# Kernel optimization log

Hardware: AMD Instinct MI355X
Metric: run time of the kernel (lower is better)

Reference implementation:

```python
import jax, jax.numpy as jnp
import numpy as np

N_NODES = 50000
N_EDGES = 400000
F_IN = 70
E_DIM = 4
HID = 128
HEADS = 4


def _add_self_loops(src, dst, edge_attr, n):
    # PyG GATConv(add_self_loops=True, fill_value='mean' when edge_dim is set):
    # self-loop edge_attr = per-dst-node mean of incoming edge_attr.
    cnt = jax.ops.segment_sum(jnp.ones((src.shape[0],), edge_attr.dtype), dst, n)
    loop_attr = jax.ops.segment_sum(edge_attr, dst, n) / jnp.clip(cnt, 1.0)[:, None]
    loop = jnp.arange(n, dtype=src.dtype)
    return (jnp.concatenate([src, loop]), jnp.concatenate([dst, loop]),
            jnp.concatenate([edge_attr, loop_attr], axis=0))


def _gat_layer(x, src, dst, e_attr, W, a_src, a_dst, We, a_edge, b, concat):
    # W: [in, H*D]; a_src/a_dst/a_edge: [H, D]; We: [edge_dim, H*D]
    n = x.shape[0]
    H, D = a_src.shape
    xs = (x @ W).reshape(n, H, D)                      # [N,H,D]
    s_src = jnp.einsum('nhd,hd->nh', xs, a_src)        # [N,H]
    s_dst = jnp.einsum('nhd,hd->nh', xs, a_dst)
    ee = (e_attr @ We).reshape(-1, H, D)               # [E,H,D]
    s_edge = jnp.einsum('ehd,hd->eh', ee, a_edge)
    alpha = jax.nn.leaky_relu(s_src[src] + s_dst[dst] + s_edge, 0.2)  # [E,H]
    # segment softmax over edges grouped by destination node
    m = jax.ops.segment_max(alpha, dst, n)
    m = jnp.where(jnp.isfinite(m), m, 0.0)
    ex = jnp.exp(alpha - m[dst])
    denom = jax.ops.segment_sum(ex, dst, n)
    alpha = ex / (denom[dst] + 1e-16)
    msg = xs[src] * alpha[..., None]                   # [E,H,D] -- dominant traffic
    agg = jax.ops.segment_sum(msg, dst, n)             # [N,H,D]
    out = agg.reshape(n, H * D) if concat else agg.mean(axis=1)
    return out + b


def _layer_norm(x, g, b, eps=1e-5):
    mu = x.mean(-1, keepdims=True)
    var = ((x - mu) ** 2).mean(-1, keepdims=True)
    return (x - mu) * jax.lax.rsqrt(var + eps) * g + b


def setup_inputs() -> dict:
    key = jax.random.key(0)
    ks = jax.random.split(key, 24)
    f32 = jnp.float32
    node_features = jax.random.normal(ks[0], (N_NODES, F_IN), f32)
    edge_index = jax.random.randint(ks[1], (2, N_EDGES), 0, N_NODES, jnp.int32)
    edge_attr = jax.random.uniform(ks[2], (N_EDGES, E_DIM), f32)
    s = 0.1
    return {
        'node_features': node_features,
        'edge_index': edge_index,
        'edge_attr': edge_attr,
        'W1': jax.random.normal(ks[3], (F_IN, HEADS * HID), f32) * s,
        'as1': jax.random.normal(ks[4], (HEADS, HID), f32) * s,
        'ad1': jax.random.normal(ks[5], (HEADS, HID), f32) * s,
        'We1': jax.random.normal(ks[6], (E_DIM, HEADS * HID), f32) * s,
        'ae1': jax.random.normal(ks[7], (HEADS, HID), f32) * s,
        'b1': jnp.zeros((HEADS * HID,), f32),
        # GAT layer 2: 512 -> 128, 1 head, mean
        'W2': jax.random.normal(ks[8], (HEADS * HID, HID), f32) * s,
        'as2': jax.random.normal(ks[9], (1, HID), f32) * s,
        'ad2': jax.random.normal(ks[10], (1, HID), f32) * s,
        'We2': jax.random.normal(ks[11], (E_DIM, HID), f32) * s,
        'ae2': jax.random.normal(ks[12], (1, HID), f32) * s,
        'b2': jnp.zeros((HID,), f32),
        'ln_g': jnp.ones((HID,), f32),
        'ln_b': jnp.zeros((HID,), f32),
        'pw': jax.random.normal(ks[13], (HID, 8), f32) * s,
        'pb': jnp.zeros((8,), f32),
        'dw': jax.random.normal(ks[14], (HID, 4), f32) * s,
        'db': jnp.zeros((4,), f32),
    }


def reference(node_features, edge_index, edge_attr, W1, as1, ad1, We1, ae1, b1,
              W2, as2, ad2, We2, ae2, b2, ln_g, ln_b, pw, pb, dw, db):
    n = node_features.shape[0]
    src, dst, ea = _add_self_loops(edge_index[0], edge_index[1], edge_attr, n)
    x = jax.nn.gelu(_gat_layer(node_features, src, dst, ea, W1, as1, ad1, We1, ae1, b1, True), approximate=False)
    x = jax.nn.gelu(_gat_layer(x, src, dst, ea, W2, as2, ad2, We2, ae2, b2, False), approximate=False)
    x = _layer_norm(x, ln_g, ln_b)
    return (x @ pw + pb, x @ dw + db)
```

## Files before the change

kernel.cpp:

```cpp
#include <hip/hip_runtime.h>
#include <hip/hip_bf16.h>
#include <math.h>

#define NN 50000
#define NE 400000
#define FIN 70
#define EDIM 4
#define HIDD 128
#define NHEAD 4
constexpr int ET = NE + NN;
constexpr int KP1 = 96;
constexpr int NFP = 72;
constexpr int SCB = (NN + 255) / 256;

constexpr size_t al4(size_t x){ return (x + 3) & ~size_t(3); }
constexpr size_t CNT_O   = 0;
constexpr size_t ZEND    = al4(CNT_O + NN);
constexpr size_t CSR_O   = ZEND;
constexpr size_t BSUM_O  = al4(CSR_O + NN + 1);
constexpr size_t BOFF_O  = al4(BSUM_O + 256);
constexpr size_t EPK_O   = al4(BOFF_O + 256);
constexpr size_t EXF1_O  = al4(EPK_O + (size_t)ET*4);
constexpr size_t EXF2_O  = al4(EXF1_O + (size_t)ET*4);
constexpr size_t SS1_O   = al4(EXF2_O + ET);
constexpr size_t SD1_O   = al4(SS1_O + (size_t)NN*4);
constexpr size_t SS2_O   = al4(SD1_O + (size_t)NN*4);
constexpr size_t SD2_O   = al4(SS2_O + NN);
constexpr size_t CST_O   = al4(SD2_O + NN);
constexpr size_t W1T_O   = al4(CST_O + 2048);
constexpr size_t W2T_O   = al4(W1T_O + 4*128*KP1/2);
constexpr size_t NFB_O   = al4(W2T_O + 128*512/2);
constexpr size_t AGG_O   = al4(NFB_O + (size_t)NN*NFP/2);
constexpr size_t XS2_O   = al4(AGG_O + (size_t)4*NN*KP1/2);

constexpr int VS1 = 0;
constexpr int VD1 = 320;
constexpr int VE1 = 640;
constexpr int VE2 = 656;
constexpr int VS2 = 704;
constexpr int VD2 = 1216;

typedef short s8v __attribute__((ext_vector_type(8)));
typedef float f4v __attribute__((ext_vector_type(4)));

__device__ __forceinline__ unsigned short f2b(float v){
  __hip_bfloat16 b = __float2bfloat16(v);
  return *(unsigned short*)&b;
}
__device__ __forceinline__ float b2f(unsigned u_lo16){
  return __uint_as_float(u_lo16 << 16);
}
__device__ __forceinline__ unsigned pk2(float lo, float hi){
  return (unsigned)f2b(lo) | ((unsigned)f2b(hi) << 16);
}
__device__ __forceinline__ float lrelu(float x){ return x > 0.f ? x : 0.2f * x; }

__device__ __forceinline__ float gelu_fast(float x){
  float z = x * 0.70710678118654752440f;
  float a = fabsf(z);
  float t = 1.f / (1.f + 0.3275911f * a);
  float p = ((((1.061405429f*t - 1.453152027f)*t + 1.421413741f)*t
              - 0.284496736f)*t + 0.254829592f)*t;
  float erfv = 1.f - p * __expf(-a * a);
  erfv = copysignf(erfv, z);
  return 0.5f * x * (1.f + erfv);
}

__global__ void k_deg(const int* __restrict__ ei, int* __restrict__ cnt){
  int e = blockIdx.x * 256 + threadIdx.x;
  if (e >= NE) return;
  atomicAdd(&cnt[ei[NE + e]], 1);
}

__global__ void k_scan1(const int* __restrict__ cnt, int* __restrict__ bsum){
  __shared__ int ws[4];
  int t = threadIdx.x, lane = t & 63, w = t >> 6;
  int i = blockIdx.x * 256 + t;
  int v = (i < NN) ? cnt[i] + 1 : 0;
  for (int o = 32; o; o >>= 1) v += __shfl_down(v, o);
  if (lane == 0) ws[w] = v;
  __syncthreads();
  if (t == 0) bsum[blockIdx.x] = ws[0] + ws[1] + ws[2] + ws[3];
}

__global__ void k_scan2(const int* __restrict__ bsum, int* __restrict__ boff){
  __shared__ int ws[4];
  int t = threadIdx.x, lane = t & 63, w = t >> 6;
  int v = (t < SCB) ? bsum[t] : 0;
  int x = v;
  #pragma unroll
  for (int o = 1; o < 64; o <<= 1){ int u = __shfl_up(x, o); if (lane >= o) x += u; }
  if (lane == 63) ws[w] = x;
  __syncthreads();
  if (w == 0 && lane < 4){
    int y = ws[lane];
    #pragma unroll
    for (int o = 1; o < 4; o <<= 1){ int u = __shfl_up(y, o); if (lane >= o) y += u; }
    ws[lane] = y;
  }
  __syncthreads();
  int incl = x + (w > 0 ? ws[w - 1] : 0);
  if (t < SCB) boff[t] = incl - v;
}

__global__ void k_scan3(const int* __restrict__ cnt, const int* __restrict__ boff,
                        int* __restrict__ csr){
  __shared__ int ws[4];
  int t = threadIdx.x, lane = t & 63, w = t >> 6;
  int i = blockIdx.x * 256 + t;
  int v = (i < NN) ? cnt[i] + 1 : 0;
  int x = v;
  #pragma unroll
  for (int o = 1; o < 64; o <<= 1){ int u = __shfl_up(x, o); if (lane >= o) x += u; }
  if (lane == 63) ws[w] = x;
  __syncthreads();
  if (w == 0 && lane < 4){
    int y = ws[lane];
    #pragma unroll
    for (int o = 1; o < 4; o <<= 1){ int u = __shfl_up(y, o); if (lane >= o) y += u; }
    ws[lane] = y;
  }
  __syncthreads();
  if (i < NN) csr[i + 1] = boff[blockIdx.x] + (w > 0 ? ws[w - 1] : 0) + x;
  if (i == 0) csr[0] = 0;
}

__global__ void k_fill(const int* __restrict__ ei, const float* __restrict__ ea,
                       const int* __restrict__ csr, int* __restrict__ cnt,
                       int4* __restrict__ epk, const float* __restrict__ ss1,
                       const float* __restrict__ sd1, const float* __restrict__ C,
                       float4* __restrict__ exf){
  int e = blockIdx.x * 256 + threadIdx.x;
  if (e >= NE) return;
  int s = ei[e], d = ei[NE + e];
  int r = atomicSub(&cnt[d], 1);
  int p = csr[d] + r - 1;
  float4 a = *(const float4*)&ea[(size_t)e * 4];
  epk[p] = make_int4(s, d, (int)pk2(a.x, a.y), (int)pk2(a.z, a.w));
  float4 ssv = *(const float4*)&ss1[(size_t)s * 4];
  float4 sdv = *(const float4*)&sd1[(size_t)d * 4];
  float e0 = __expf(lrelu(ssv.x + sdv.x + a.x*C[VE1+0] + a.y*C[VE1+4] + a.z*C[VE1+8]  + a.w*C[VE1+12]));
  float e1 = __expf(lrelu(ssv.y + sdv.y + a.x*C[VE1+1] + a.y*C[VE1+5] + a.z*C[VE1+9]  + a.w*C[VE1+13]));
  float e2 = __expf(lrelu(ssv.z + sdv.z + a.x*C[VE1+2] + a.y*C[VE1+6] + a.z*C[VE1+10] + a.w*C[VE1+14]));
  float e3 = __expf(lrelu(ssv.w + sdv.w + a.x*C[VE1+3] + a.y*C[VE1+7] + a.z*C[VE1+11] + a.w*C[VE1+15]));
  exf[p] = make_float4(e0, e1, e2, e3);
}

__global__ void k_prep(const float* __restrict__ W1, const float* __restrict__ as1,
                       const float* __restrict__ ad1, const float* __restrict__ We1,
                       const float* __restrict__ ae1, const float* __restrict__ W2,
                       const float* __restrict__ as2, const float* __restrict__ ad2,
                       const float* __restrict__ We2, const float* __restrict__ ae2,
                       float* __restrict__ C){
  int t = threadIdx.x;
  if (t < 280){
    int k = t >> 2, h = t & 3;
    float s = 0.f, d = 0.f;
    for (int dd = 0; dd < 128; ++dd){
      float w = W1[k*512 + h*128 + dd];
      s += w * as1[h*128 + dd];
      d += w * ad1[h*128 + dd];
    }
    C[VS1 + t] = s; C[VD1 + t] = d;
  }
  if (t < 16){
    int k = t >> 2, h = t & 3;
    float s = 0.f;
    for (int dd = 0; dd < 128; ++dd) s += We1[k*512 + h*128 + dd] * ae1[h*128 + dd];
    C[VE1 + t] = s;
  }
  if (t < 4){
    float s = 0.f;
    for (int dd = 0; dd < 128; ++dd) s += We2[t*128 + dd] * ae2[dd];
    C[VE2 + t] = s;
  }
  {
    float s = 0.f, d = 0.f;
    for (int dd = 0; dd < 128; ++dd){
      float w = W2[t*128 + dd];
      s += w * as2[dd];
      d += w * ad2[dd];
    }
    C[VS2 + t] = s; C[VD2 + t] = d;
  }
}

__global__ void k_tw(const float* __restrict__ W1, const float* __restrict__ W2,
                     unsigned short* __restrict__ W1p, unsigned short* __restrict__ W2p){
  int i = blockIdx.x * 256 + threadIdx.x;
  if (i < 12*128*32){
    int kk = i & 31, r = (i >> 5) & 127, ph = i >> 12;
    int h = ph / 3, kf = ph - 3*h;
    int kg = kf*32 + kk;
    float v = (kg < FIN) ? W1[kg*512 + h*128 + r] : 0.f;
    W1p[i] = f2b(v);
  } else {
    int j = i - 12*128*32;
    if (j < 16*128*32){
      int kk = j & 31, r = (j >> 5) & 127, p = j >> 12;
      W2p[j] = f2b(W2[(p*32 + kk)*128 + r]);
    }
  }
}

__global__ __launch_bounds__(256) void k_cnfs1(const float* __restrict__ nf,
    const float* __restrict__ C, unsigned short* __restrict__ nfb,
    float* __restrict__ ss1, float* __restrict__ sd1){
  int lane = threadIdx.x & 63, w = threadIdx.x >> 6;
  int n = blockIdx.x * 4 + w;
  if (n >= NN) return;
  int c0 = lane * 2;
  bool act = lane < 35;
  float v0 = 0.f, v1 = 0.f;
  if (act){
    v0 = nf[(size_t)n * FIN + c0];
    v1 = nf[(size_t)n * FIN + c0 + 1];
  }
  if (lane < 36) *(unsigned*)&nfb[(size_t)n * NFP + c0] = act ? pk2(v0, v1) : 0u;
  float sh[4] = {0,0,0,0}, dh[4] = {0,0,0,0};
  if (act){
    float4 cs0 = *(const float4*)&C[VS1 + c0*4];
    float4 cs1 = *(const float4*)&C[VS1 + (c0+1)*4];
    float4 cd0 = *(const float4*)&C[VD1 + c0*4];
    float4 cd1 = *(const float4*)&C[VD1 + (c0+1)*4];
    sh[0] = v0*cs0.x + v1*cs1.x; sh[1] = v0*cs0.y + v1*cs1.y;
    sh[2] = v0*cs0.z + v1*cs1.z; sh[3] = v0*cs0.w + v1*cs1.w;
    dh[0] = v0*cd0.x + v1*cd1.x; dh[1] = v0*cd0.y + v1*cd1.y;
    dh[2] = v0*cd0.z + v1*cd1.z; dh[3] = v0*cd0.w + v1*cd1.w;
  }
  #pragma unroll
  for (int o = 32; o; o >>= 1){
    #pragma unroll
    for (int h = 0; h < 4; ++h){
      sh[h] += __shfl_xor(sh[h], o);
      dh[h] += __shfl_xor(dh[h], o);
    }
  }
  if (lane == 0){
    *(float4*)&ss1[(size_t)n*4] = make_float4(sh[0], sh[1], sh[2], sh[3]);
    *(float4*)&sd1[(size_t)n*4] = make_float4(dh[0], dh[1], dh[2], dh[3]);
  }
}

__global__ __launch_bounds__(256, 4) void k_gemm12(
    const unsigned short* __restrict__ agg, const unsigned short* __restrict__ W1p,
    const unsigned short* __restrict__ W2p, const float* __restrict__ b1,
    const float* __restrict__ Cv, unsigned short* __restrict__ xs2b,
    float* __restrict__ ss2, float* __restrict__ sd2){
  __shared__ unsigned short xt[32 * 516];
  __shared__ float ssp[32][4], sdp[32][4];
  int tid = threadIdx.x, lane = tid & 63, wn = tid >> 6;
  int m15 = lane & 15, rq = lane >> 4;
  int r0 = blockIdx.x * 32;
  int gr0 = r0 + m15;      if (gr0 >= NN) gr0 = NN - 1;
  int gr1 = r0 + 16 + m15; if (gr1 >= NN) gr1 = NN - 1;
  float s2a0 = 0.f, s2d0 = 0.f, s2a1 = 0.f, s2d1 = 0.f;
  constexpr size_t HS = (size_t)NN * KP1;
  const int bfo = (wn * 32 + m15) * 32 + rq * 8;
  const unsigned short* A0 = agg + (size_t)gr0 * KP1 + rq * 8;
  const unsigned short* A1 = agg + (size_t)gr1 * KP1 + rq * 8;

  #pragma unroll
  for (int h = 0; h < 4; ++h){
    f4v acc[2][2] = {};
    const unsigned short* Bh = W1p + h * 3 * 4096 + bfo;
    #pragma unroll
    for (int kf = 0; kf < 3; ++kf){
      s8v a0 = *(const s8v*)(A0 + (size_t)h * HS + kf * 32);
      s8v a1 = *(const s8v*)(A1 + (size_t)h * HS + kf * 32);
      #pragma unroll
      for (int ni = 0; ni < 2; ++ni){
        s8v bf = *(const s8v*)(Bh + kf * 4096 + ni * 512);
        acc[0][ni] = __builtin_amdgcn_mfma_f32_16x16x32_bf16(bf, a0, acc[0][ni], 0, 0, 0);
        acc[1][ni] = __builtin_amdgcn_mfma_f32_16x16x32_bf16(bf, a1, acc[1][ni], 0, 0, 0);
      }
    }
    #pragma unroll
    for (int m = 0; m < 2; ++m){
      #pragma unroll
      for (int ni = 0; ni < 2; ++ni){
        int cb = h * 128 + wn * 32 + ni * 16 + rq * 4;
        float4 bv = *(const float4*)&b1[cb];
        float v0 = gelu_fast(acc[m][ni][0] + bv.x);
        float v1 = gelu_fast(acc[m][ni][1] + bv.y);
        float v2 = gelu_fast(acc[m][ni][2] + bv.z);
        float v3 = gelu_fast(acc[m][ni][3] + bv.w);
        float4 cs = *(const float4*)&Cv[VS2 + cb];
        float4 cd = *(const float4*)&Cv[VD2 + cb];
        float pa = v0*cs.x + v1*cs.y + v2*cs.z + v3*cs.w;
        float pd = v0*cd.x + v1*cd.y + v2*cd.z + v3*cd.w;
        if (m == 0){ s2a0 += pa; s2d0 += pd; } else { s2a1 += pa; s2d1 += pd; }
        *(uint2*)&xt[(m * 16 + m15) * 516 + cb] = make_uint2(pk2(v0, v1), pk2(v2, v3));
      }
    }
  }
  s2a0 += __shfl_xor(s2a0, 16); s2a0 += __shfl_xor(s2a0, 32);
  s2d0 += __shfl_xor(s2d0, 16); s2d0 += __shfl_xor(s2d0, 32);
  s2a1 += __shfl_xor(s2a1, 16); s2a1 += __shfl_xor(s2a1, 32);
  s2d1 += __shfl_xor(s2d1, 16); s2d1 += __shfl_xor(s2d1, 32);
  if (rq == 0){
    ssp[m15][wn] = s2a0;      sdp[m15][wn] = s2d0;
    ssp[16 + m15][wn] = s2a1; sdp[16 + m15][wn] = s2d1;
  }

  __syncthreads();

  if (tid < 32 && r0 + tid < NN){
    ss2[r0 + tid] = (ssp[tid][0] + ssp[tid][1]) + (ssp[tid][2] + ssp[tid][3]);
    sd2[r0 + tid] = (sdp[tid][0] + sdp[tid][1]) + (sdp[tid][2] + sdp[tid][3]);
  }

  f4v acc2[2][2] = {};
  #pragma unroll
  for (int p = 0; p < 16; ++p){
    s8v x0 = *(const s8v*)&xt[m15 * 516 + p * 32 + rq * 8];
    s8v x1 = *(const s8v*)&xt[(16 + m15) * 516 + p * 32 + rq * 8];
    #pragma unroll
    for (int ni = 0; ni < 2; ++ni){
      s8v bf = *(const s8v*)(W2p + p * 4096 + bfo + ni * 512);
      acc2[0][ni] = __builtin_amdgcn_mfma_f32_16x16x32_bf16(bf, x0, acc2[0][ni], 0, 0, 0);
      acc2[1][ni] = __builtin_amdgcn_mfma_f32_16x16x32_bf16(bf, x1, acc2[1][ni], 0, 0, 0);
    }
  }
  #pragma unroll
  for (int m = 0; m < 2; ++m){
    int grow = r0 + m * 16 + m15;
    if (grow < NN){
      #pragma unroll
      for (int ni = 0; ni < 2; ++ni){
        int gc = wn * 32 + ni * 16 + rq * 4;
        *(uint2*)&xs2b[(size_t)grow * 128 + gc] =
            make_uint2(pk2(acc2[m][ni][0], acc2[m][ni][1]),
                       pk2(acc2[m][ni][2], acc2[m][ni][3]));
      }
    }
  }
}

__global__ __launch_bounds__(256) void k_aggnf(const int* __restrict__ csr,
    int4* __restrict__ epk, const float4* __restrict__ exf,
    const unsigned short* __restrict__ nfb, const float* __restrict__ ss1,
    const float* __restrict__ sd1, const float* __restrict__ Cv,
    unsigned short* __restrict__ agg){
  int lane = threadIdx.x & 63, w = threadIdx.x >> 6;
  int n = blockIdx.x * 4 + w;
  if (n >= NN) return;
  int off = __builtin_amdgcn_readfirstlane(csr[n]);
  int end = __builtin_amdgcn_readfirstlane(csr[n + 1]);
  int endr = end - 1;
  int col = lane * 2;
  bool act = lane < 36;
  float d0=0,d1=0,d2=0,d3=0;
  float a00=0,a01=0,a10=0,a11=0,a20=0,a21=0,a30=0,a31=0;
  float t0=0,t1=0,t2=0,t3=0;
  int p = off;
  for (; p + 4 <= endr; p += 4){
    int4 q0 = epk[p], q1 = epk[p+1], q2 = epk[p+2], q3 = epk[p+3];
    float4 e0 = exf[p], e1 = exf[p+1], e2 = exf[p+2], e3 = exf[p+3];
    unsigned u0 = 0, u1 = 0, u2 = 0, u3 = 0;
    if (act){
      u0 = *(const unsigned*)&nfb[(size_t)q0.x * NFP + col];
      u1 = *(const unsigned*)&nfb[(size_t)q1.x * NFP + col];
      u2 = *(const unsigned*)&nfb[(size_t)q2.x * NFP + col];
      u3 = *(const unsigned*)&nfb[(size_t)q3.x * NFP + col];
    }
    t0 += (b2f((unsigned)q0.z & 0xffffu) + b2f((unsigned)q1.z & 0xffffu))
        + (b2f((unsigned)q2.z & 0xffffu) + b2f((unsigned)q3.z & 0xffffu));
    t1 += (b2f((unsigned)q0.z >> 16) + b2f((unsigned)q1.z >> 16))
        + (b2f((unsigned)q2.z >> 16) + b2f((unsigned)q3.z >> 16));
    t2 += (b2f((unsigned)q0.w & 0xffffu) + b2f((unsigned)q1.w & 0xffffu))
        + (b2f((unsigned)q2.w & 0xffffu) + b2f((unsigned)q3.w & 0xffffu));
    t3 += (b2f((unsigned)q0.w >> 16) + b2f((unsigned)q1.w >> 16))
        + (b2f((unsigned)q2.w >> 16) + b2f((unsigned)q3.w >> 16));
    d0 += (e0.x + e1.x) + (e2.x + e3.x);
    d1 += (e0.y + e1.y) + (e2.y + e3.y);
    d2 += (e0.z + e1.z) + (e2.z + e3.z);
    d3 += (e0.w + e1.w) + (e2.w + e3.w);
    float v00 = b2f(u0 & 0xffffu), v01 = b2f(u0 >> 16);
    float v10 = b2f(u1 & 0xffffu), v11 = b2f(u1 >> 16);
    float v20 = b2f(u2 & 0xffffu), v21 = b2f(u2 >> 16);
    float v30 = b2f(u3 & 0xffffu), v31 = b2f(u3 >> 16);
    a00 += (e0.x*v00 + e1.x*v10) + (e2.x*v20 + e3.x*v30);
    a01 += (e0.x*v01 + e1.x*v11) + (e2.x*v21 + e3.x*v31);
    a10 += (e0.y*v00 + e1.y*v10) + (e2.y*v20 + e3.y*v30);
    a11 += (e0.y*v01 + e1.y*v11) + (e2.y*v21 + e3.y*v31);
    a20 += (e0.z*v00 + e1.z*v10) + (e2.z*v20 + e3.z*v30);
    a21 += (e0.z*v01 + e1.z*v11) + (e2.z*v21 + e3.z*v31);
    a30 += (e0.w*v00 + e1.w*v10) + (e2.w*v20 + e3.w*v30);
    a31 += (e0.w*v01 + e1.w*v11) + (e2.w*v21 + e3.w*v31);
  }
  for (; p + 2 <= endr; p += 2){
    int4 q0 = epk[p], q1 = epk[p+1];
    float4 e0 = exf[p], e1 = exf[p+1];
    unsigned u0 = 0, u1 = 0;
    if (act){
      u0 = *(const unsigned*)&nfb[(size_t)q0.x * NFP + col];
      u1 = *(const unsigned*)&nfb[(size_t)q1.x * NFP + col];
    }
    t0 += b2f((unsigned)q0.z & 0xffffu) + b2f((unsigned)q1.z & 0xffffu);
    t1 += b2f((unsigned)q0.z >> 16)     + b2f((unsigned)q1.z >> 16);
    t2 += b2f((unsigned)q0.w & 0xffffu) + b2f((unsigned)q1.w & 0xffffu);
    t3 += b2f((unsigned)q0.w >> 16)     + b2f((unsigned)q1.w >> 16);
    d0 += e0.x + e1.x; d1 += e0.y + e1.y; d2 += e0.z + e1.z; d3 += e0.w + e1.w;
    float v00 = b2f(u0 & 0xffffu), v01 = b2f(u0 >> 16);
    float v10 = b2f(u1 & 0xffffu), v11 = b2f(u1 >> 16);
    a00 += e0.x*v00 + e1.x*v10; a01 += e0.x*v01 + e1.x*v11;
    a10 += e0.y*v00 + e1.y*v10; a11 += e0.y*v01 + e1.y*v11;
    a20 += e0.z*v00 + e1.z*v10; a21 += e0.z*v01 + e1.z*v11;
    a30 += e0.w*v00 + e1.w*v10; a31 += e0.w*v01 + e1.w*v11;
  }
  if (p < endr){
    int4 q0 = epk[p];
    float4 e0 = exf[p];
    unsigned u0 = 0;
    if (act) u0 = *(const unsigned*)&nfb[(size_t)q0.x * NFP + col];
    t0 += b2f((unsigned)q0.z & 0xffffu); t1 += b2f((unsigned)q0.z >> 16);
    t2 += b2f((unsigned)q0.w & 0xffffu); t3 += b2f((unsigned)q0.w >> 16);
    d0 += e0.x; d1 += e0.y; d2 += e0.z; d3 += e0.w;
    float v00 = b2f(u0 & 0xffffu), v01 = b2f(u0 >> 16);
    a00 += e0.x*v00; a01 += e0.x*v01;
    a10 += e0.y*v00; a11 += e0.y*v01;
    a20 += e0.z*v00; a21 += e0.z*v01;
    a30 += e0.w*v00; a31 += e0.w*v01;
  }
  int deg = endr - off;
  float inv = 1.f / (float)(deg > 1 ? deg : 1);
  float m0 = t0*inv, m1 = t1*inv, m2 = t2*inv, m3 = t3*inv;
  if (lane == 0) epk[endr] = make_int4(n, n, (int)pk2(m0, m1), (int)pk2(m2, m3));
  float4 ssv = *(const float4*)&ss1[(size_t)n * 4];
  float4 sdn = *(const float4*)&sd1[(size_t)n * 4];
  float e0 = __expf(lrelu(ssv.x + sdn.x + m0*Cv[VE1+0] + m1*Cv[VE1+4] + m2*Cv[VE1+8]  + m3*Cv[VE1+12]));
  float e1 = __expf(lrelu(ssv.y + sdn.y + m0*Cv[VE1+1] + m1*Cv[VE1+5] + m2*Cv[VE1+9]  + m3*Cv[VE1+13]));
  float e2 = __expf(lrelu(ssv.z + sdn.z + m0*Cv[VE1+2] + m1*Cv[VE1+6] + m2*Cv[VE1+10] + m3*Cv[VE1+14]));
  float e3 = __expf(lrelu(ssv.w + sdn.w + m0*Cv[VE1+3] + m1*Cv[VE1+7] + m2*Cv[VE1+11] + m3*Cv[VE1+15]));
  {
    unsigned us = act ? *(const unsigned*)&nfb[(size_t)n * NFP + col] : 0u;
    float v0 = b2f(us & 0xffffu), v1 = b2f(us >> 16);
    d0 += e0; d1 += e1; d2 += e2; d3 += e3;
    a00 += e0*v0; a01 += e0*v1;
    a10 += e1*v0; a11 += e1*v1;
    a20 += e2*v0; a21 += e2*v1;
    a30 += e3*v0; a31 += e3*v1;
  }
  float i0 = 1.f/(d0+1e-16f), i1 = 1.f/(d1+1e-16f);
  float i2 = 1.f/(d2+1e-16f), i3 = 1.f/(d3+1e-16f);
  constexpr size_t HS = (size_t)NN * KP1;
  size_t base = (size_t)n * KP1 + col;
  if (act){
    *(unsigned*)&agg[base]        = pk2(a00*i0, a01*i0);
    *(unsigned*)&agg[base +   HS] = pk2(a10*i1, a11*i1);
    *(unsigned*)&agg[base + 2*HS] = pk2(a20*i2, a21*i2);
    *(unsigned*)&agg[base + 3*HS] = pk2(a30*i3, a31*i3);
  } else if (lane < 48){
    *(unsigned*)&agg[base]        = 0u;
    *(unsigned*)&agg[base +   HS] = 0u;
    *(unsigned*)&agg[base + 2*HS] = 0u;
    *(unsigned*)&agg[base + 3*HS] = 0u;
  }
}

__global__ __launch_bounds__(256) void k_agg2(
    const int* __restrict__ csr, const int4* __restrict__ epk,
    const float* __restrict__ ss2, const float* __restrict__ sd2,
    const float* __restrict__ Cv, const unsigned short* __restrict__ xs2b,
    const float* __restrict__ b2, const float* __restrict__ lng,
    const float* __restrict__ lnb, const float* __restrict__ pw,
    const float* __restrict__ pb, const float* __restrict__ dwm,
    const float* __restrict__ dbv, float* __restrict__ out){
  int lane = threadIdx.x & 63, w = threadIdx.x >> 6;
  int n = blockIdx.x * 4 + w;
  if (n >= NN) return;
  int off = __builtin_amdgcn_readfirstlane(csr[n]);
  int end = __builtin_amdgcn_readfirstlane(csr[n + 1]);
  float sd2n = sd2[n];
  float cv0 = Cv[VE2], cv1 = Cv[VE2+1], cv2 = Cv[VE2+2], cv3 = Cv[VE2+3];
  int c0 = lane * 2;
  float acc0 = 0.f, acc1 = 0.f, den = 0.f;
  int p = off;
  for (; p + 4 <= end; p += 4){
    int4 p0 = epk[p], p1 = epk[p+1], p2 = epk[p+2], p3 = epk[p+3];
    int s0 = p0.x, s1 = p1.x, s2 = p2.x, s3 = p3.x;
    float sv0 = ss2[s0], sv1 = ss2[s1], sv2 = ss2[s2], sv3 = ss2[s3];
    unsigned u0 = *(const unsigned*)&xs2b[(size_t)s0 * 128 + c0];
    unsigned u1 = *(const unsigned*)&xs2b[(size_t)s1 * 128 + c0];
    unsigned u2 = *(const unsigned*)&xs2b[(size_t)s2 * 128 + c0];
    unsigned u3 = *(const unsigned*)&xs2b[(size_t)s3 * 128 + c0];
    float e0 = __expf(lrelu(sv0 + sd2n
             + b2f((unsigned)p0.z & 0xffffu)*cv0 + b2f((unsigned)p0.z >> 16)*cv1
             + b2f((unsigned)p0.w & 0xffffu)*cv2 + b2f((unsigned)p0.w >> 16)*cv3));
    float e1 = __expf(lrelu(sv1 + sd2n
             + b2f((unsigned)p1.z & 0xffffu)*cv0 + b2f((unsigned)p1.z >> 16)*cv1
             + b2f((unsigned)p1.w & 0xffffu)*cv2 + b2f((unsigned)p1.w >> 16)*cv3));
    float e2 = __expf(lrelu(sv2 + sd2n
             + b2f((unsigned)p2.z & 0xffffu)*cv0 + b2f((unsigned)p2.z >> 16)*cv1
             + b2f((unsigned)p2.w & 0xffffu)*cv2 + b2f((unsigned)p2.w >> 16)*cv3));
    float e3 = __expf(lrelu(sv3 + sd2n
             + b2f((unsigned)p3.z & 0xffffu)*cv0 + b2f((unsigned)p3.z >> 16)*cv1
             + b2f((unsigned)p3.w & 0xffffu)*cv2 + b2f((unsigned)p3.w >> 16)*cv3));
    den += (e0 + e1) + (e2 + e3);
    acc0 += (e0*b2f(u0 & 0xffffu) + e1*b2f(u1 & 0xffffu))
          + (e2*b2f(u2 & 0xffffu) + e3*b2f(u3 & 0xffffu));
    acc1 += (e0*b2f(u0 >> 16) + e1*b2f(u1 >> 16))
          + (e2*b2f(u2 >> 16) + e3*b2f(u3 >> 16));
  }
  for (; p + 2 <= end; p += 2){
    int4 p0 = epk[p], p1 = epk[p+1];
    int s0 = p0.x, s1 = p1.x;
    float sv0 = ss2[s0], sv1 = ss2[s1];
    unsigned u0 = *(const unsigned*)&xs2b[(size_t)s0 * 128 + c0];
    unsigned u1 = *(const unsigned*)&xs2b[(size_t)s1 * 128 + c0];
    float e0 = __expf(lrelu(sv0 + sd2n
             + b2f((unsigned)p0.z & 0xffffu)*cv0 + b2f((unsigned)p0.z >> 16)*cv1
             + b2f((unsigned)p0.w & 0xffffu)*cv2 + b2f((unsigned)p0.w >> 16)*cv3));
    float e1 = __expf(lrelu(sv1 + sd2n
             + b2f((unsigned)p1.z & 0xffffu)*cv0 + b2f((unsigned)p1.z >> 16)*cv1
             + b2f((unsigned)p1.w & 0xffffu)*cv2 + b2f((unsigned)p1.w >> 16)*cv3));
    den += e0 + e1;
    acc0 += e0*b2f(u0 & 0xffffu) + e1*b2f(u1 & 0xffffu);
    acc1 += e0*b2f(u0 >> 16) + e1*b2f(u1 >> 16);
  }
  if (p < end){
    int4 p0 = epk[p];
    int s0 = p0.x;
    float sv0 = ss2[s0];
    unsigned u0 = *(const unsigned*)&xs2b[(size_t)s0 * 128 + c0];
    float e0 = __expf(lrelu(sv0 + sd2n
             + b2f((unsigned)p0.z & 0xffffu)*cv0 + b2f((unsigned)p0.z >> 16)*cv1
             + b2f((unsigned)p0.w & 0xffffu)*cv2 + b2f((unsigned)p0.w >> 16)*cv3));
    den += e0;
    acc0 += e0*b2f(u0 & 0xffffu);
    acc1 += e0*b2f(u0 >> 16);
  }
  float invd = 1.f / (den + 1e-16f);
  float g0 = gelu_fast(acc0 * invd + b2[c0]);
  float g1 = gelu_fast(acc1 * invd + b2[c0 + 1]);
  float s = g0 + g1;
  #pragma unroll
  for (int o = 32; o; o >>= 1) s += __shfl_xor(s, o);
  float mu = s * (1.f / 128.f);
  float e0 = g0 - mu, e1 = g1 - mu;
  float q = e0*e0 + e1*e1;
  #pragma unroll
  for (int o = 32; o; o >>= 1) q += __shfl_xor(q, o);
  float rstd = rsqrtf(q * (1.f / 128.f) + 1e-5f);
  float y0 = e0 * rstd * lng[c0] + lnb[c0];
  float y1 = e1 * rstd * lng[c0 + 1] + lnb[c0 + 1];
  float pr[12];
  #pragma unroll
  for (int jj = 0; jj < 8; ++jj) pr[jj] = y0 * pw[c0*8 + jj] + y1 * pw[(c0+1)*8 + jj];
  #pragma unroll
  for (int jj = 0; jj < 4; ++jj) pr[8+jj] = y0 * dwm[c0*4 + jj] + y1 * dwm[(c0+1)*4 + jj];
  #pragma unroll
  for (int o = 32; o; o >>= 1)
    #pragma unroll
    for (int jj = 0; jj < 12; ++jj) pr[jj] += __shfl_xor(pr[jj], o);
  if (lane == 0){
    #pragma unroll
    for (int jj = 0; jj < 8; ++jj) out[(size_t)n*8 + jj] = pr[jj] + pb[jj];
    #pragma unroll
    for (int jj = 0; jj < 4; ++jj) out[(size_t)NN*8 + (size_t)n*4 + jj] = pr[8+jj] + dbv[jj];
  }
}

extern "C" void kernel_launch(void* const* d_in, const int* in_sizes, int n_in,
                              void* d_out, int out_size, void* d_ws, size_t ws_size,
                              hipStream_t stream){
  const float* nf  = (const float*)d_in[0];
  const int*   ei  = (const int*)  d_in[1];
  const float* ea  = (const float*)d_in[2];
  const float* W1  = (const float*)d_in[3];
  const float* as1 = (const float*)d_in[4];
  const float* ad1 = (const float*)d_in[5];
  const float* We1 = (const float*)d_in[6];
  const float* ae1 = (const float*)d_in[7];
  const float* b1  = (const float*)d_in[8];
  const float* W2  = (const float*)d_in[9];
  const float* as2 = (const float*)d_in[10];
  const float* ad2 = (const float*)d_in[11];
  const float* We2 = (const float*)d_in[12];
  const float* ae2 = (const float*)d_in[13];
  const float* b2  = (const float*)d_in[14];
  const float* lng = (const float*)d_in[15];
  const float* lnb = (const float*)d_in[16];
  const float* pw  = (const float*)d_in[17];
  const float* pb  = (const float*)d_in[18];
  const float* dw  = (const float*)d_in[19];
  const float* db  = (const float*)d_in[20];
  float* out = (float*)d_out;

  float* wf = (float*)d_ws;
  int*      cnt  = (int*)     (wf + CNT_O);
  int*      csr  = (int*)     (wf + CSR_O);
  int*      bsum = (int*)     (wf + BSUM_O);
  int*      boff = (int*)     (wf + BOFF_O);
  int4*     epk  = (int4*)    (wf + EPK_O);
  float4*   exf1 = (float4*)  (wf + EXF1_O);
  float*    ss1  =            (wf + SS1_O);
  float*    sd1  =            (wf + SD1_O);
  float*    ss2  =            (wf + SS2_O);
  float*    sd2  =            (wf + SD2_O);
  float*    Cc   =            (wf + CST_O);
  unsigned short* W1p = (unsigned short*)(wf + W1T_O);
  unsigned short* W2p = (unsigned short*)(wf + W2T_O);
  unsigned short* nfb = (unsigned short*)(wf + NFB_O);
  unsigned short* agg = (unsigned short*)(wf + AGG_O);
  unsigned short* xs2b= (unsigned short*)(wf + XS2_O);

  hipMemsetAsync(cnt, 0, NN * sizeof(int), stream);
  k_prep<<<1, 512, 0, stream>>>(W1, as1, ad1, We1, ae1, W2, as2, ad2, We2, ae2, Cc);
  k_tw<<<(12*128*32 + 16*128*32 + 255) / 256, 256, 0, stream>>>(W1, W2, W1p, W2p);
  k_cnfs1<<<(NN + 3) / 4, 256, 0, stream>>>(nf, Cc, nfb, ss1, sd1);
  k_deg<<<(NE + 255) / 256, 256, 0, stream>>>(ei, cnt);
  k_scan1<<<SCB, 256, 0, stream>>>(cnt, bsum);
  k_scan2<<<1, 256, 0, stream>>>(bsum, boff);
  k_scan3<<<SCB, 256, 0, stream>>>(cnt, boff, csr);
  k_fill<<<(NE + 255) / 256, 256, 0, stream>>>(ei, ea, csr, cnt, epk, ss1, sd1, Cc, exf1);
  k_aggnf<<<(NN + 3) / 4, 256, 0, stream>>>(csr, epk, exf1, nfb, ss1, sd1, Cc, agg);
  k_gemm12<<<(NN + 31) / 32, 256, 0, stream>>>(agg, W1p, W2p, b1, Cc, xs2b, ss2, sd2);
  k_agg2<<<(NN + 3) / 4, 256, 0, stream>>>(csr, epk, ss2, sd2, Cc, xs2b,
                                           b2, lng, lnb, pw, pb, dw, db, out);
}
```

Baseline: 338.7 us.

## Fuse setup kernels and record per-edge rank to drop fill atomics

Merges weight transpose, attention-constant precompute and the count zeroing into one launch, replacing a memset and two kernels. Folds the degree-count kernel into the node-feature kernel as extra blocks and stores each edge's atomicAdd return value as a rank. The fill kernel then computes its CSR slot from csr plus rank with no second atomic pass. This cuts launch count and atomic traffic at the cost of an extra per-edge int array. The precompute block now runs 512 logical threads in a loop inside a 256-thread block.

```diff
diff --git a/kernel.cpp b/kernel.cpp
--- a/kernel.cpp
+++ b/kernel.cpp
@@ -21,8 +21,8 @@
 constexpr size_t BOFF_O  = al4(BSUM_O + 256);
 constexpr size_t EPK_O   = al4(BOFF_O + 256);
 constexpr size_t EXF1_O  = al4(EPK_O + (size_t)ET*4);
-constexpr size_t EXF2_O  = al4(EXF1_O + (size_t)ET*4);
-constexpr size_t SS1_O   = al4(EXF2_O + ET);
+constexpr size_t RNK_O   = al4(EXF1_O + (size_t)ET*4);
+constexpr size_t SS1_O   = al4(RNK_O + ET);
 constexpr size_t SD1_O   = al4(SS1_O + (size_t)NN*4);
 constexpr size_t SS2_O   = al4(SD1_O + (size_t)NN*4);
 constexpr size_t SD2_O   = al4(SS2_O + NN);
@@ -40,6 +40,10 @@
 constexpr int VS2 = 704;
 constexpr int VD2 = 1216;
 
+constexpr int TW_BLK = (12*128*32 + 16*128*32) / 256;
+constexpr int CN_BLK = (NN + 3) / 4;
+constexpr int DG_BLK = (NE + 255) / 256;
+
 typedef short s8v __attribute__((ext_vector_type(8)));
 typedef float f4v __attribute__((ext_vector_type(4)));
 
@@ -66,148 +70,80 @@
   return 0.5f * x * (1.f + erfv);
 }
 
-__global__ void k_deg(const int* __restrict__ ei, int* __restrict__ cnt){
-  int e = blockIdx.x * 256 + threadIdx.x;
-  if (e >= NE) return;
-  atomicAdd(&cnt[ei[NE + e]], 1);
-}
-
-__global__ void k_scan1(const int* __restrict__ cnt, int* __restrict__ bsum){
-  __shared__ int ws[4];
-  int t = threadIdx.x, lane = t & 63, w = t >> 6;
-  int i = blockIdx.x * 256 + t;
-  int v = (i < NN) ? cnt[i] + 1 : 0;
-  for (int o = 32; o; o >>= 1) v += __shfl_down(v, o);
-  if (lane == 0) ws[w] = v;
-  __syncthreads();
-  if (t == 0) bsum[blockIdx.x] = ws[0] + ws[1] + ws[2] + ws[3];
-}
-
-__global__ void k_scan2(const int* __restrict__ bsum, int* __restrict__ boff){
-  __shared__ int ws[4];
-  int t = threadIdx.x, lane = t & 63, w = t >> 6;
-  int v = (t < SCB) ? bsum[t] : 0;
-  int x = v;
-  #pragma unroll
-  for (int o = 1; o < 64; o <<= 1){ int u = __shfl_up(x, o); if (lane >= o) x += u; }
-  if (lane == 63) ws[w] = x;
-  __syncthreads();
-  if (w == 0 && lane < 4){
-    int y = ws[lane];
-    #pragma unroll
-    for (int o = 1; o < 4; o <<= 1){ int u = __shfl_up(y, o); if (lane >= o) y += u; }
-    ws[lane] = y;
-  }
-  __syncthreads();
-  int incl = x + (w > 0 ? ws[w - 1] : 0);
-  if (t < SCB) boff[t] = incl - v;
-}
-
-__global__ void k_scan3(const int* __restrict__ cnt, const int* __restrict__ boff,
-                        int* __restrict__ csr){
-  __shared__ int ws[4];
-  int t = threadIdx.x, lane = t & 63, w = t >> 6;
-  int i = blockIdx.x * 256 + t;
-  int v = (i < NN) ? cnt[i] + 1 : 0;
-  int x = v;
-  #pragma unroll
-  for (int o = 1; o < 64; o <<= 1){ int u = __shfl_up(x, o); if (lane >= o) x += u; }
-  if (lane == 63) ws[w] = x;
-  __syncthreads();
-  if (w == 0 && lane < 4){
-    int y = ws[lane];
-    #pragma unroll
-    for (int o = 1; o < 4; o <<= 1){ int u = __shfl_up(y, o); if (lane >= o) y += u; }
-    ws[lane] = y;
-  }
-  __syncthreads();
-  if (i < NN) csr[i + 1] = boff[blockIdx.x] + (w > 0 ? ws[w - 1] : 0) + x;
-  if (i == 0) csr[0] = 0;
-}
-
-__global__ void k_fill(const int* __restrict__ ei, const float* __restrict__ ea,
-                       const int* __restrict__ csr, int* __restrict__ cnt,
-                       int4* __restrict__ epk, const float* __restrict__ ss1,
-                       const float* __restrict__ sd1, const float* __restrict__ C,
-                       float4* __restrict__ exf){
-  int e = blockIdx.x * 256 + threadIdx.x;
-  if (e >= NE) return;
-  int s = ei[e], d = ei[NE + e];
-  int r = atomicSub(&cnt[d], 1);
-  int p = csr[d] + r - 1;
-  float4 a = *(const float4*)&ea[(size_t)e * 4];
-  epk[p] = make_int4(s, d, (int)pk2(a.x, a.y), (int)pk2(a.z, a.w));
-  float4 ssv = *(const float4*)&ss1[(size_t)s * 4];
-  float4 sdv = *(const float4*)&sd1[(size_t)d * 4];
-  float e0 = __expf(lrelu(ssv.x + sdv.x + a.x*C[VE1+0] + a.y*C[VE1+4] + a.z*C[VE1+8]  + a.w*C[VE1+12]));
-  float e1 = __expf(lrelu(ssv.y + sdv.y + a.x*C[VE1+1] + a.y*C[VE1+5] + a.z*C[VE1+9]  + a.w*C[VE1+13]));
-  float e2 = __expf(lrelu(ssv.z + sdv.z + a.x*C[VE1+2] + a.y*C[VE1+6] + a.z*C[VE1+10] + a.w*C[VE1+14]));
-  float e3 = __expf(lrelu(ssv.w + sdv.w + a.x*C[VE1+3] + a.y*C[VE1+7] + a.z*C[VE1+11] + a.w*C[VE1+15]));
-  exf[p] = make_float4(e0, e1, e2, e3);
-}
-
-__global__ void k_prep(const float* __restrict__ W1, const float* __restrict__ as1,
-                       const float* __restrict__ ad1, const float* __restrict__ We1,
-                       const float* __restrict__ ae1, const float* __restrict__ W2,
-                       const float* __restrict__ as2, const float* __restrict__ ad2,
-                       const float* __restrict__ We2, const float* __restrict__ ae2,
-                       float* __restrict__ C){
-  int t = threadIdx.x;
-  if (t < 280){
-    int k = t >> 2, h = t & 3;
-    float s = 0.f, d = 0.f;
-    for (int dd = 0; dd < 128; ++dd){
-      float w = W1[k*512 + h*128 + dd];
-      s += w * as1[h*128 + dd];
-      d += w * ad1[h*128 + dd];
-    }
-    C[VS1 + t] = s; C[VD1 + t] = d;
-  }
-  if (t < 16){
-    int k = t >> 2, h = t & 3;
-    float s = 0.f;
-    for (int dd = 0; dd < 128; ++dd) s += We1[k*512 + h*128 + dd] * ae1[h*128 + dd];
-    C[VE1 + t] = s;
-  }
-  if (t < 4){
-    float s = 0.f;
-    for (int dd = 0; dd < 128; ++dd) s += We2[t*128 + dd] * ae2[dd];
-    C[VE2 + t] = s;
-  }
-  {
-    float s = 0.f, d = 0.f;
-    for (int dd = 0; dd < 128; ++dd){
-      float w = W2[t*128 + dd];
-      s += w * as2[dd];
-      d += w * ad2[dd];
-    }
-    C[VS2 + t] = s; C[VD2 + t] = d;
-  }
-}
-
-__global__ void k_tw(const float* __restrict__ W1, const float* __restrict__ W2,
-                     unsigned short* __restrict__ W1p, unsigned short* __restrict__ W2p){
-  int i = blockIdx.x * 256 + threadIdx.x;
-  if (i < 12*128*32){
-    int kk = i & 31, r = (i >> 5) & 127, ph = i >> 12;
-    int h = ph / 3, kf = ph - 3*h;
-    int kg = kf*32 + kk;
-    float v = (kg < FIN) ? W1[kg*512 + h*128 + r] : 0.f;
-    W1p[i] = f2b(v);
-  } else {
-    int j = i - 12*128*32;
-    if (j < 16*128*32){
+__global__ void k_ptw(const float* __restrict__ W1, const float* __restrict__ as1,
+                      const float* __restrict__ ad1, const float* __restrict__ We1,
+                      const float* __restrict__ ae1, const float* __restrict__ W2,
+                      const float* __restrict__ as2, const float* __restrict__ ad2,
+                      const float* __restrict__ We2, const float* __restrict__ ae2,
+                      float* __restrict__ C, unsigned short* __restrict__ W1p,
+                      unsigned short* __restrict__ W2p, int* __restrict__ cnt){
+  int bid = blockIdx.x, tid = threadIdx.x;
+  if (bid < TW_BLK){
+    int i = bid * 256 + tid;
+    if (i < 12*128*32){
+      int kk = i & 31, r = (i >> 5) & 127, ph = i >> 12;
+      int h = ph / 3, kf = ph - 3*h;
+      int kg = kf*32 + kk;
+      float v = (kg < FIN) ? W1[kg*512 + h*128 + r] : 0.f;
+      W1p[i] = f2b(v);
+    } else {
+      int j = i - 12*128*32;
       int kk = j & 31, r = (j >> 5) & 127, p = j >> 12;
       W2p[j] = f2b(W2[(p*32 + kk)*128 + r]);
     }
-  }
+    return;
+  }
+  if (bid == TW_BLK){
+    for (int t = tid; t < 512; t += 256){
+      if (t < 280){
+        int k = t >> 2, h = t & 3;
+        float s = 0.f, d = 0.f;
+        for (int dd = 0; dd < 128; ++dd){
+          float w = W1[k*512 + h*128 + dd];
+          s += w * as1[h*128 + dd];
+          d += w * ad1[h*128 + dd];
+        }
+        C[VS1 + t] = s; C[VD1 + t] = d;
+      }
+      if (t < 16){
+        int k = t >> 2, h = t & 3;
+        float s = 0.f;
+        for (int dd = 0; dd < 128; ++dd) s += We1[k*512 + h*128 + dd] * ae1[h*128 + dd];
+        C[VE1 + t] = s;
+      }
+      if (t < 4){
+        float s = 0.f;
+        for (int dd = 0; dd < 128; ++dd) s += We2[t*128 + dd] * ae2[dd];
+        C[VE2 + t] = s;
+      }
+      {
+        float s = 0.f, d = 0.f;
+        for (int dd = 0; dd < 128; ++dd){
+          float w = W2[t*128 + dd];
+          s += w * as2[dd];
+          d += w * ad2[dd];
+        }
+        C[VS2 + t] = s; C[VD2 + t] = d;
+      }
+    }
+    return;
+  }
+  int i = (bid - TW_BLK - 1) * 256 + tid;
+  if (i < NN) cnt[i] = 0;
 }
 
 __global__ __launch_bounds__(256) void k_cnfs1(const float* __restrict__ nf,
     const float* __restrict__ C, unsigned short* __restrict__ nfb,
-    float* __restrict__ ss1, float* __restrict__ sd1){
+    float* __restrict__ ss1, float* __restrict__ sd1,
+    const int* __restrict__ ei, int* __restrict__ cnt, int* __restrict__ rnk){
+  int bid = blockIdx.x;
+  if (bid >= CN_BLK){
+    int e = (bid - CN_BLK) * 256 + threadIdx.x;
+    if (e < NE) rnk[e] = atomicAdd(&cnt[ei[NE + e]], 1);
+    return;
+  }
   int lane = threadIdx.x & 63, w = threadIdx.x >> 6;
-  int n = blockIdx.x * 4 + w;
+  int n = bid * 4 + w;
   if (n >= NN) return;
   int c0 = lane * 2;
   bool act = lane < 35;
@@ -240,6 +176,79 @@
     *(float4*)&ss1[(size_t)n*4] = make_float4(sh[0], sh[1], sh[2], sh[3]);
     *(float4*)&sd1[(size_t)n*4] = make_float4(dh[0], dh[1], dh[2], dh[3]);
   }
+}
+
+__global__ void k_scan1(const int* __restrict__ cnt, int* __restrict__ bsum){
+  __shared__ int ws[4];
+  int t = threadIdx.x, lane = t & 63, w = t >> 6;
+  int i = blockIdx.x * 256 + t;
+  int v = (i < NN) ? cnt[i] + 1 : 0;
+  for (int o = 32; o; o >>= 1) v += __shfl_down(v, o);
+  if (lane == 0) ws[w] = v;
+  __syncthreads();
+  if (t == 0) bsum[blockIdx.x] = ws[0] + ws[1] + ws[2] + ws[3];
+}
+
+__global__ void k_scan2(const int* __restrict__ bsum, int* __restrict__ boff){
+  __shared__ int ws[4];
+  int t = threadIdx.x, lane = t & 63, w = t >> 6;
+  int v = (t < SCB) ? bsum[t] : 0;
+  int x = v;
+  #pragma unroll
+  for (int o = 1; o < 64; o <<= 1){ int u = __shfl_up(x, o); if (lane >= o) x += u; }
+  if (lane == 63) ws[w] = x;
+  __syncthreads();
+  if (w == 0 && lane < 4){
+    int y = ws[lane];
+    #pragma unroll
+    for (int o = 1; o < 4; o <<= 1){ int u = __shfl_up(y, o); if (lane >= o) y += u; }
+    ws[lane] = y;
+  }
+  __syncthreads();
+  int incl = x + (w > 0 ? ws[w - 1] : 0);
+  if (t < SCB) boff[t] = incl - v;
+}
+
+__global__ void k_scan3(const int* __restrict__ cnt, const int* __restrict__ boff,
+                        int* __restrict__ csr){
+  __shared__ int ws[4];
+  int t = threadIdx.x, lane = t & 63, w = t >> 6;
+  int i = blockIdx.x * 256 + t;
+  int v = (i < NN) ? cnt[i] + 1 : 0;
+  int x = v;
+  #pragma unroll
+  for (int o = 1; o < 64; o <<= 1){ int u = __shfl_up(x, o); if (lane >= o) x += u; }
+  if (lane == 63) ws[w] = x;
+  __syncthreads();
+  if (w == 0 && lane < 4){
+    int y = ws[lane];
+    #pragma unroll
+    for (int o = 1; o < 4; o <<= 1){ int u = __shfl_up(y, o); if (lane >= o) y += u; }
+    ws[lane] = y;
+  }
+  __syncthreads();
+  if (i < NN) csr[i + 1] = boff[blockIdx.x] + (w > 0 ? ws[w - 1] : 0) + x;
+  if (i == 0) csr[0] = 0;
+}
+
+__global__ void k_fill(const int* __restrict__ ei, const float* __restrict__ ea,
+                       const int* __restrict__ csr, const int* __restrict__ rnk,
+                       int4* __restrict__ epk, const float* __restrict__ ss1,
+                       const float* __restrict__ sd1, const float* __restrict__ C,
+                       float4* __restrict__ exf){
+  int e = blockIdx.x * 256 + threadIdx.x;
+  if (e >= NE) return;
+  int s = ei[e], d = ei[NE + e];
+  int p = csr[d] + rnk[e];
+  float4 a = *(const float4*)&ea[(size_t)e * 4];
+  epk[p] = make_int4(s, d, (int)pk2(a.x, a.y), (int)pk2(a.z, a.w));
+  float4 ssv = *(const float4*)&ss1[(size_t)s * 4];
+  float4 sdv = *(const float4*)&sd1[(size_t)d * 4];
+  float e0 = __expf(lrelu(ssv.x + sdv.x + a.x*C[VE1+0] + a.y*C[VE1+4] + a.z*C[VE1+8]  + a.w*C[VE1+12]));
+  float e1 = __expf(lrelu(ssv.y + sdv.y + a.x*C[VE1+1] + a.y*C[VE1+5] + a.z*C[VE1+9]  + a.w*C[VE1+13]));
+  float e2 = __expf(lrelu(ssv.z + sdv.z + a.x*C[VE1+2] + a.y*C[VE1+6] + a.z*C[VE1+10] + a.w*C[VE1+14]));
+  float e3 = __expf(lrelu(ssv.w + sdv.w + a.x*C[VE1+3] + a.y*C[VE1+7] + a.z*C[VE1+11] + a.w*C[VE1+15]));
+  exf[p] = make_float4(e0, e1, e2, e3);
 }
 
 __global__ __launch_bounds__(256, 4) void k_gemm12(
@@ -595,6 +604,7 @@
   int*      boff = (int*)     (wf + BOFF_O);
   int4*     epk  = (int4*)    (wf + EPK_O);
   float4*   exf1 = (float4*)  (wf + EXF1_O);
+  int*      rnk  = (int*)     (wf + RNK_O);
   float*    ss1  =            (wf + SS1_O);
   float*    sd1  =            (wf + SD1_O);
   float*    ss2  =            (wf + SS2_O);
@@ -606,15 +616,14 @@
   unsigned short* agg = (unsigned short*)(wf + AGG_O);
   unsigned short* xs2b= (unsigned short*)(wf + XS2_O);
 
-  hipMemsetAsync(cnt, 0, NN * sizeof(int), stream);
-  k_prep<<<1, 512, 0, stream>>>(W1, as1, ad1, We1, ae1, W2, as2, ad2, We2, ae2, Cc);
-  k_tw<<<(12*128*32 + 16*128*32 + 255) / 256, 256, 0, stream>>>(W1, W2, W1p, W2p);
-  k_cnfs1<<<(NN + 3) / 4, 256, 0, stream>>>(nf, Cc, nfb, ss1, sd1);
-  k_deg<<<(NE + 255) / 256, 256, 0, stream>>>(ei, cnt);
+  k_ptw<<<TW_BLK + 1 + SCB, 256, 0, stream>>>(W1, as1, ad1, We1, ae1,
+                                              W2, as2, ad2, We2, ae2,
+                                              Cc, W1p, W2p, cnt);
+  k_cnfs1<<<CN_BLK + DG_BLK, 256, 0, stream>>>(nf, Cc, nfb, ss1, sd1, ei, cnt, rnk);
   k_scan1<<<SCB, 256, 0, stream>>>(cnt, bsum);
   k_scan2<<<1, 256, 0, stream>>>(bsum, boff);
   k_scan3<<<SCB, 256, 0, stream>>>(cnt, boff, csr);
-  k_fill<<<(NE + 255) / 256, 256, 0, stream>>>(ei, ea, csr, cnt, epk, ss1, sd1, Cc, exf1);
+  k_fill<<<(NE + 255) / 256, 256, 0, stream>>>(ei, ea, csr, rnk, epk, ss1, sd1, Cc, exf1);
   k_aggnf<<<(NN + 3) / 4, 256, 0, stream>>>(csr, epk, exf1, nfb, ss1, sd1, Cc, agg);
   k_gemm12<<<(NN + 31) / 32, 256, 0, stream>>>(agg, W1p, W2p, b1, Cc, xs2b, ss2, sd2);
   k_agg2<<<(NN + 3) / 4, 256, 0, stream>>>(csr, epk, ss2, sd2, Cc, xs2b,
```

Measured after the change: 325.8 us (median of 3 runs). 3.8% less time.
